# Optimization experiments

Hardware: AMD Instinct MI355X
Metric: run time of the kernel (lower is better)

Reference implementation:

```python
import jax, jax.numpy as jnp
import numpy as np

D_MODEL = 1024
N_HEADS = 16
D_HEAD = D_MODEL // N_HEADS
SCALE = D_HEAD ** -0.5


def setup_inputs() -> dict:
    key = jax.random.key(0)
    ks = jax.random.split(key, 9)
    s = 0.02
    x = jax.random.normal(ks[0], (2, 2048, D_MODEL), dtype=jnp.float32)
    Wq = jax.random.normal(ks[1], (D_MODEL, D_MODEL), dtype=jnp.float32) * s
    Wk = jax.random.normal(ks[2], (D_MODEL, D_MODEL), dtype=jnp.float32) * s
    Wv = jax.random.normal(ks[3], (D_MODEL, D_MODEL), dtype=jnp.float32) * s
    Wo = jax.random.normal(ks[4], (D_MODEL, D_MODEL), dtype=jnp.float32) * s
    bq = jax.random.normal(ks[5], (D_MODEL,), dtype=jnp.float32) * s
    bk = jax.random.normal(ks[6], (D_MODEL,), dtype=jnp.float32) * s
    bv = jax.random.normal(ks[7], (D_MODEL,), dtype=jnp.float32) * s
    bo = jax.random.normal(ks[8], (D_MODEL,), dtype=jnp.float32) * s
    return {"x": x, "Wq": Wq, "bq": bq, "Wk": Wk, "bk": bk,
            "Wv": Wv, "bv": bv, "Wo": Wo, "bo": bo}


def reference(x, Wq, bq, Wk, bk, Wv, bv, Wo, bo):
    B, S, _ = x.shape
    # torch nn.Linear: y = x @ W.T + b
    def proj(W, b):
        h = jnp.einsum('bsd,ed->bse', x, W) + b
        return h.reshape(B, S, N_HEADS, D_HEAD).transpose(0, 2, 1, 3)  # [B,H,S,Dh]
    Q = proj(Wq, bq)
    K = proj(Wk, bk)
    V = proj(Wv, bv)
    # chunked QK^T softmax over full K == full attention (no mask, dropout=0)
    scores = jnp.einsum('bhqd,bhkd->bhqk', Q, K) * SCALE  # [B,H,S,S]
    attn = jax.nn.softmax(scores, axis=-1)
    out = jnp.einsum('bhqk,bhkd->bhqd', attn, V)
    out = out.transpose(0, 2, 1, 3).reshape(B, S, D_MODEL)
    return jnp.einsum('bsd,ed->bse', out, Wo) + bo
```

## Files before the change

### kernel.cpp

```cpp
#include <hip/hip_runtime.h>
#include <cstdint>
#include <cstddef>


typedef unsigned short u16;
typedef unsigned int u32;
typedef __bf16 bf16x8 __attribute__((ext_vector_type(8)));
typedef float f32x4 __attribute__((ext_vector_type(4)));

#define GLOAD_LDS16(gp, lp)                                                            \
  __builtin_amdgcn_global_load_lds((const __attribute__((address_space(1))) void*)(gp),\
                                   (__attribute__((address_space(3))) void*)(lp),      \
                                   16, 0, 0)

__device__ __forceinline__ u16 f2bf(float f) {
  unsigned u = __builtin_bit_cast(unsigned, f);
  u = u + 0x7fffu + ((u >> 16) & 1u);
  return (u16)(u >> 16);
}

__device__ __forceinline__ u32 cvtpk(float a, float b) {
  u32 r;
  asm("v_cvt_pk_bf16_f32 %0, %1, %2" : "=v"(r) : "v"(a), "v"(b));
  return r;
}

#define QSCALE 0.1803368801111204f

__global__ void cvt_all(const float* __restrict__ x,
                        const float* __restrict__ wq, const float* __restrict__ wk,
                        const float* __restrict__ wv, const float* __restrict__ wo,
                        u16* __restrict__ xb, u16* __restrict__ wqb,
                        u16* __restrict__ wkb, u16* __restrict__ wvb,
                        u16* __restrict__ wob) {
  int bx = blockIdx.x;
  const float* s; u16* d; int off;
  if (bx < 2048)      { s = x;  d = xb;  off = bx; }
  else if (bx < 2560) { s = wq; d = wqb; off = bx - 2048; }
  else if (bx < 3072) { s = wk; d = wkb; off = bx - 2560; }
  else if (bx < 3584) { s = wv; d = wvb; off = bx - 3072; }
  else                { s = wo; d = wob; off = bx - 3584; }
  int i = off * 2048 + threadIdx.x * 8;
  float4 a = *(const float4*)(s + i);
  float4 b = *(const float4*)(s + i + 4);
  uint4 o;
  o.x = f2bf(a.x) | ((u32)f2bf(a.y) << 16);
  o.y = f2bf(a.z) | ((u32)f2bf(a.w) << 16);
  o.z = f2bf(b.x) | ((u32)f2bf(b.y) << 16);
  o.w = f2bf(b.z) | ((u32)f2bf(b.w) << 16);
  *(uint4*)(d + i) = o;
}

template <int MODE, int BM, int BN>
__global__ __launch_bounds__(256, MODE == 0 ? 3 : 4) void gemm_mfma(
    const u16* __restrict__ A,
    const u16* __restrict__ W0, const u16* __restrict__ W1, const u16* __restrict__ W2,
    const float* __restrict__ b0, const float* __restrict__ b1, const float* __restrict__ b2,
    u16* __restrict__ o0, u16* __restrict__ o1, u16* __restrict__ o2,
    float* __restrict__ oF)
{
  constexpr int MF = BM / 32;
  constexpr int NF = BN / 32;
  constexpr int AG = BM / 32;
  constexpr int BG = BN / 32;
  constexpr int NY = (MODE == 0) ? 32 : 64;
  constexpr int TOT = (MODE == 0) ? 24 * 32 : 16 * 64;

  __shared__ __align__(16) u16 As[BM * 64];
  __shared__ __align__(16) u16 Bs[BN * 64];

  const int tid = threadIdx.x;
  const int w = tid >> 6, l = tid & 63;
  const int lane = l & 15, quad = l >> 4;
  const int wm = w >> 1, wn = w & 1;

  const int idb = blockIdx.y * gridDim.x + blockIdx.x;
  const int lid = (idb & 7) * (TOT >> 3) + (idb >> 3);
  const int m0 = (lid % NY) * BM;
  const int n0g = (lid / NY) * BN;

  const int src = (MODE == 0) ? (n0g >> 10) : 0;
  const u16* Wsel = (MODE == 0) ? (src == 0 ? W0 : (src == 1 ? W1 : W2)) : W0;
  const float* bsel = (MODE == 0) ? (src == 0 ? b0 : (src == 1 ? b1 : b2)) : b0;
  const int n_base = (MODE == 0) ? (n0g & 1023) : n0g;

  const int c8 = ((l & 7) ^ (l >> 3)) * 8;
  const int lrow = l >> 3;

  f32x4 acc[MF][NF] = {};

  for (int kt = 0; kt < 1024; kt += 64) {
    __syncthreads();
    const u16* Ag = A + (size_t)m0 * 1024 + kt;
    const u16* Bg = Wsel + (size_t)n_base * 1024 + kt;
    #pragma unroll
    for (int i = 0; i < AG; ++i) {
      int rr = w * (8 * AG) + i * 8;
      GLOAD_LDS16(Ag + (size_t)(rr + lrow) * 1024 + c8, As + rr * 64);
    }
    #pragma unroll
    for (int i = 0; i < BG; ++i) {
      int rr = w * (8 * BG) + i * 8;
      GLOAD_LDS16(Bg + (size_t)(rr + lrow) * 1024 + c8, Bs + rr * 64);
    }
    __syncthreads();

    bf16x8 af[MF][2], bf[NF][2];
    #pragma unroll
    for (int mf = 0; mf < MF; ++mf)
      #pragma unroll
      for (int ks = 0; ks < 2; ++ks)
        af[mf][ks] = *(const bf16x8*)((const char*)As +
            (wm * (BM / 2) + mf * 16 + lane) * 128 + (((ks * 4 + quad) ^ (lane & 7)) * 16));
    #pragma unroll
    for (int nf = 0; nf < NF; ++nf)
      #pragma unroll
      for (int ks = 0; ks < 2; ++ks)
        bf[nf][ks] = *(const bf16x8*)((const char*)Bs +
            (wn * (BN / 2) + nf * 16 + lane) * 128 + (((ks * 4 + quad) ^ (lane & 7)) * 16));
    #pragma unroll
    for (int ks = 0; ks < 2; ++ks)
      #pragma unroll
      for (int mf = 0; mf < MF; ++mf)
        #pragma unroll
        for (int nf = 0; nf < NF; ++nf)
          acc[mf][nf] = __builtin_amdgcn_mfma_f32_16x16x32_bf16(
              af[mf][ks], bf[nf][ks], acc[mf][nf], 0, 0, 0);
  }

  float bb[NF];
  #pragma unroll
  for (int nf = 0; nf < NF; ++nf)
    bb[nf] = bsel[n_base + wn * (BN / 2) + nf * 16 + lane];

  u16* osel = (MODE == 0) ? (src == 0 ? o0 : (src == 1 ? o1 : o2)) : o0;

  #pragma unroll
  for (int mf = 0; mf < MF; ++mf) {
    int mb = m0 + wm * (BM / 2) + mf * 16 + quad * 4;
    #pragma unroll
    for (int nf = 0; nf < NF; ++nf) {
      int n_l = wn * (BN / 2) + nf * 16 + lane;
      if (MODE == 0 && src != 1) {
        float sc = (src == 0) ? QSCALE : 1.0f;
        float v0 = (acc[mf][nf][0] + bb[nf]) * sc;
        float v1 = (acc[mf][nf][1] + bb[nf]) * sc;
        float v2 = (acc[mf][nf][2] + bb[nf]) * sc;
        float v3 = (acc[mf][nf][3] + bb[nf]) * sc;
        int bi = mb >> 11, s = mb & 2047;
        int n_in = n_base + n_l;
        int h = n_in >> 6, dh = n_in & 63;
        uint2 pk = make_uint2(cvtpk(v0, v1), cvtpk(v2, v3));
        *(uint2*)(osel + (((size_t)(bi * 16 + h) * 64 + dh) * 2048 + s)) = pk;
      } else {
        #pragma unroll
        for (int r = 0; r < 4; ++r) {
          float v = acc[mf][nf][r] + bb[nf];
          int m = mb + r;
          if (MODE == 0) {
            int bi = m >> 11, s = m & 2047;
            int n_in = n_base + n_l;
            int h = n_in >> 6, dh = n_in & 63;
            osel[(((size_t)(bi * 16 + h) * 2048 + s) << 6) + dh] = f2bf(v);
          } else {
            oF[(size_t)m * 1024 + n0g + n_l] = v;
          }
        }
      }
    }
  }
}

union SMemU {
  struct {
    u16 K[3][64 * 64];
    u16 V[3][64 * 64];
  } m;
  struct {
    float O[4][32 * 64];
    float L[4][32];
  } f;
};

__global__ __launch_bounds__(512, 4) void attn_mfma(
    const u16* __restrict__ Qg_, const u16* __restrict__ Kg_,
    const u16* __restrict__ VTg_, u16* __restrict__ Og)
{
  __shared__ __align__(16) SMemU sm;

  const int tid = threadIdx.x;
  const int w = tid >> 6, l = tid & 63;
  const int lane = l & 15, quad = l >> 4;
  const int g = w >> 1;
  const int kh = w & 1;

  const int idb = blockIdx.y * 16 + blockIdx.x;
  const int lid = (idb & 7) * 64 + (idb >> 3);
  const int bh = lid >> 4;
  const int q0 = (lid & 15) * 128;

  const u16* QTg = Qg_ + (size_t)bh * 64 * 2048;
  const u16* Kg  = Kg_ + (size_t)bh * 2048 * 64;
  const u16* VTg = VTg_ + (size_t)bh * 64 * 2048;

  const int c8 = ((l & 7) ^ (l >> 3)) * 8;
  const int lrow = l >> 3;
  const int rr = w * 8;

  const int qcol = q0 + g * 32 + lane;
  bf16x8 bq[2][2];
  #pragma unroll
  for (int qf = 0; qf < 2; ++qf)
    #pragma unroll
    for (int ks = 0; ks < 2; ++ks) {
      bf16x8 v;
      #pragma unroll
      for (int j = 0; j < 8; ++j)
        v[j] = __builtin_bit_cast(__bf16,
            QTg[(size_t)(ks * 32 + quad * 8 + j) * 2048 + qcol + qf * 16]);
      bq[qf][ks] = v;
    }

  GLOAD_LDS16(Kg + (size_t)(rr + lrow) * 64 + c8, sm.m.K[0] + rr * 64);
  GLOAD_LDS16(VTg + (size_t)(rr + lrow) * 2048 + c8, sm.m.V[0] + rr * 64);
  GLOAD_LDS16(Kg + (size_t)(64 + rr + lrow) * 64 + c8, sm.m.K[1] + rr * 64);
  GLOAD_LDS16(VTg + (size_t)(rr + lrow) * 2048 + 64 + c8, sm.m.V[1] + rr * 64);

  f32x4 oa[2][4] = {};
  float lsum[2] = {0.f, 0.f};
  int cur = 0;

  for (int kt = 0; kt < 32; ++kt) {
    if (kt < 31) asm volatile("s_waitcnt vmcnt(2)" ::: "memory");
    else         asm volatile("s_waitcnt vmcnt(0)" ::: "memory");
    __builtin_amdgcn_s_barrier();
    asm volatile("" ::: "memory");

    if (kt < 30) {
      int pf = (cur == 0) ? 2 : cur - 1;
      GLOAD_LDS16(Kg + (size_t)((kt + 2) * 64 + rr + lrow) * 64 + c8,
                  sm.m.K[pf] + rr * 64);
      GLOAD_LDS16(VTg + (size_t)(rr + lrow) * 2048 + (kt + 2) * 64 + c8,
                  sm.m.V[pf] + rr * 64);
    }

    f32x4 sa[2][2] = {};
    #pragma unroll
    for (int ks = 0; ks < 2; ++ks) {
      bf16x8 ak[2];
      #pragma unroll
      for (int kf = 0; kf < 2; ++kf)
        ak[kf] = *(const bf16x8*)((const char*)sm.m.K[cur] +
            (kh * 32 + kf * 16 + lane) * 128 + (((ks * 4 + quad) ^ (lane & 7)) * 16));
      #pragma unroll
      for (int kf = 0; kf < 2; ++kf)
        #pragma unroll
        for (int qf = 0; qf < 2; ++qf)
          sa[kf][qf] = __builtin_amdgcn_mfma_f32_16x16x32_bf16(
              ak[kf], bq[qf][ks], sa[kf][qf], 0, 0, 0);
    }

    bf16x8 ap[2];
    #pragma unroll
    for (int qf = 0; qf < 2; ++qf) {
      float x0 = __builtin_amdgcn_exp2f(sa[0][qf][0]);
      float x1 = __builtin_amdgcn_exp2f(sa[0][qf][1]);
      float x2 = __builtin_amdgcn_exp2f(sa[0][qf][2]);
      float x3 = __builtin_amdgcn_exp2f(sa[0][qf][3]);
      float y0 = __builtin_amdgcn_exp2f(sa[1][qf][0]);
      float y1 = __builtin_amdgcn_exp2f(sa[1][qf][1]);
      float y2 = __builtin_amdgcn_exp2f(sa[1][qf][2]);
      float y3 = __builtin_amdgcn_exp2f(sa[1][qf][3]);
      lsum[qf] += ((x0 + x1) + (x2 + x3)) + ((y0 + y1) + (y2 + y3));
      u32 X0 = cvtpk(x0, x1), X1 = cvtpk(x2, x3);
      u32 Y0 = cvtpk(y0, y1), Y1 = cvtpk(y2, y3);
      asm("v_permlane32_swap_b32 %0, %1" : "+v"(X0), "+v"(Y0));
      asm("v_permlane16_swap_b32 %0, %1" : "+v"(X0), "+v"(Y0));
      asm("v_permlane32_swap_b32 %0, %1" : "+v"(X1), "+v"(Y1));
      asm("v_permlane16_swap_b32 %0, %1" : "+v"(X1), "+v"(Y1));
      uint4 d4 = make_uint4(X0, X1, Y0, Y1);
      ap[qf] = __builtin_bit_cast(bf16x8, d4);
    }

    {
      bf16x8 bv[4];
      #pragma unroll
      for (int df = 0; df < 4; ++df)
        bv[df] = *(const bf16x8*)((const char*)sm.m.V[cur] +
            (df * 16 + lane) * 128 + (((kh * 4 + quad) ^ (lane & 7)) * 16));
      #pragma unroll
      for (int qf = 0; qf < 2; ++qf)
        #pragma unroll
        for (int df = 0; df < 4; ++df)
          oa[qf][df] = __builtin_amdgcn_mfma_f32_16x16x32_bf16(
              ap[qf], bv[df], oa[qf][df], 0, 0, 0);
    }

    cur = (cur == 2) ? 0 : cur + 1;
  }

  #pragma unroll
  for (int qf = 0; qf < 2; ++qf) {
    lsum[qf] += __shfl_xor(lsum[qf], 16);
    lsum[qf] += __shfl_xor(lsum[qf], 32);
  }

  __syncthreads();
  if (kh == 1) {
    #pragma unroll
    for (int qf = 0; qf < 2; ++qf)
      #pragma unroll
      for (int df = 0; df < 4; ++df)
        #pragma unroll
        for (int r = 0; r < 4; ++r)
          sm.f.O[g][(qf * 16 + quad * 4 + r) * 64 + df * 16 + lane] = oa[qf][df][r];
    if (l < 16) {
      sm.f.L[g][l] = lsum[0];
      sm.f.L[g][16 + l] = lsum[1];
    }
  }
  __syncthreads();
  if (kh == 0) {
    const int b = bh >> 4, hh = bh & 15;
    u16* Ob = Og + ((size_t)b * 2048 + q0 + g * 32) * 1024 + hh * 64;
    float ltot[2];
    #pragma unroll
    for (int qf = 0; qf < 2; ++qf)
      ltot[qf] = lsum[qf] + sm.f.L[g][qf * 16 + lane];
    #pragma unroll
    for (int qf = 0; qf < 2; ++qf)
      #pragma unroll
      for (int r = 0; r < 4; ++r) {
        float inv = 1.0f / __shfl(ltot[qf], quad * 4 + r, 16);
        int qrow = qf * 16 + quad * 4 + r;
        #pragma unroll
        for (int df = 0; df < 4; ++df) {
          float v = oa[qf][df][r] + sm.f.O[g][qrow * 64 + df * 16 + lane];
          Ob[(size_t)qrow * 1024 + df * 16 + lane] = f2bf(v * inv);
        }
      }
  }
}

extern "C" void kernel_launch(void* const* d_in, const int* in_sizes, int n_in,
                              void* d_out, int out_size, void* d_ws, size_t ws_size,
                              hipStream_t stream)
{
  (void)in_sizes; (void)n_in; (void)out_size; (void)ws_size;
  const float* x  = (const float*)d_in[0];
  const float* Wq = (const float*)d_in[1];
  const float* bq = (const float*)d_in[2];
  const float* Wk = (const float*)d_in[3];
  const float* bk = (const float*)d_in[4];
  const float* Wv = (const float*)d_in[5];
  const float* bv = (const float*)d_in[6];
  const float* Wo = (const float*)d_in[7];
  const float* bo = (const float*)d_in[8];
  float* y = (float*)d_out;

  const size_t NM = (size_t)4096 * 1024;
  u16* xb  = (u16*)d_ws;
  u16* wqb = xb + NM;
  u16* wkb = wqb + 1024 * 1024;
  u16* wvb = wkb + 1024 * 1024;
  u16* wob = wvb + 1024 * 1024;
  u16* Qb  = wob + 1024 * 1024;
  u16* Kb  = Qb + NM;
  u16* VTb = Kb + NM;
  u16* AOb = VTb + NM;

  cvt_all<<<4096, 256, 0, stream>>>(x, Wq, Wk, Wv, Wo, xb, wqb, wkb, wvb, wob);

  gemm_mfma<0, 128, 128><<<dim3(24, 32), 256, 0, stream>>>(
      xb, wqb, wkb, wvb, bq, bk, bv, Qb, Kb, VTb, nullptr);

  attn_mfma<<<dim3(16, 32), 512, 0, stream>>>(Qb, Kb, VTb, AOb);

  gemm_mfma<1, 64, 64><<<dim3(16, 64), 256, 0, stream>>>(
      AOb, wob, nullptr, nullptr, bo, nullptr, nullptr,
      nullptr, nullptr, nullptr, y);
}
```

Before: 179.0 us.

## Double-buffer LDS tiles in GEMM to overlap global loads with MFMA

The projection GEMM kernel now keeps two LDS buffers for the A and B tiles. It issues the global-to-LDS loads for the next K tile before computing on the current one, so there is one barrier per iteration instead of two. This is meant to hide global memory latency behind the MFMA work. It doubles the LDS footprint, and the QKV mode's occupancy hint drops from 3 to 2 blocks per CU to match.

```diff
diff --git a/kernel.cpp b/kernel.cpp
--- a/kernel.cpp
+++ b/kernel.cpp
@@ -52,7 +52,7 @@
 }
 
 template <int MODE, int BM, int BN>
-__global__ __launch_bounds__(256, MODE == 0 ? 3 : 4) void gemm_mfma(
+__global__ __launch_bounds__(256, MODE == 0 ? 2 : 4) void gemm_mfma(
     const u16* __restrict__ A,
     const u16* __restrict__ W0, const u16* __restrict__ W1, const u16* __restrict__ W2,
     const float* __restrict__ b0, const float* __restrict__ b1, const float* __restrict__ b2,
@@ -65,9 +65,10 @@
   constexpr int BG = BN / 32;
   constexpr int NY = (MODE == 0) ? 32 : 64;
   constexpr int TOT = (MODE == 0) ? 24 * 32 : 16 * 64;
-
-  __shared__ __align__(16) u16 As[BM * 64];
-  __shared__ __align__(16) u16 Bs[BN * 64];
+  constexpr int NT = 16;
+
+  __shared__ __align__(16) u16 As[2][BM * 64];
+  __shared__ __align__(16) u16 Bs[2][BN * 64];
 
   const int tid = threadIdx.x;
   const int w = tid >> 6, l = tid & 63;
@@ -87,36 +88,47 @@
   const int c8 = ((l & 7) ^ (l >> 3)) * 8;
   const int lrow = l >> 3;
 
-  f32x4 acc[MF][NF] = {};
-
-  for (int kt = 0; kt < 1024; kt += 64) {
-    __syncthreads();
-    const u16* Ag = A + (size_t)m0 * 1024 + kt;
-    const u16* Bg = Wsel + (size_t)n_base * 1024 + kt;
+  const u16* Ag0 = A + (size_t)m0 * 1024;
+  const u16* Bg0 = Wsel + (size_t)n_base * 1024;
+
+  auto stage = [&](int buf, int kt) {
+    const u16* Ag = Ag0 + kt * 64;
+    const u16* Bg = Bg0 + kt * 64;
     #pragma unroll
     for (int i = 0; i < AG; ++i) {
       int rr = w * (8 * AG) + i * 8;
-      GLOAD_LDS16(Ag + (size_t)(rr + lrow) * 1024 + c8, As + rr * 64);
+      GLOAD_LDS16(Ag + (size_t)(rr + lrow) * 1024 + c8, As[buf] + rr * 64);
     }
     #pragma unroll
     for (int i = 0; i < BG; ++i) {
       int rr = w * (8 * BG) + i * 8;
-      GLOAD_LDS16(Bg + (size_t)(rr + lrow) * 1024 + c8, Bs + rr * 64);
-    }
-    __syncthreads();
+      GLOAD_LDS16(Bg + (size_t)(rr + lrow) * 1024 + c8, Bs[buf] + rr * 64);
+    }
+  };
+
+  f32x4 acc[MF][NF] = {};
+
+  stage(0, 0);
+  asm volatile("s_waitcnt vmcnt(0)" ::: "memory");
+  __builtin_amdgcn_s_barrier();
+  asm volatile("" ::: "memory");
+
+  for (int kt = 0; kt < NT; ++kt) {
+    const int cur = kt & 1;
+    if (kt < NT - 1) stage(cur ^ 1, kt + 1);
 
     bf16x8 af[MF][2], bf[NF][2];
     #pragma unroll
     for (int mf = 0; mf < MF; ++mf)
       #pragma unroll
       for (int ks = 0; ks < 2; ++ks)
-        af[mf][ks] = *(const bf16x8*)((const char*)As +
+        af[mf][ks] = *(const bf16x8*)((const char*)As[cur] +
             (wm * (BM / 2) + mf * 16 + lane) * 128 + (((ks * 4 + quad) ^ (lane & 7)) * 16));
     #pragma unroll
     for (int nf = 0; nf < NF; ++nf)
       #pragma unroll
       for (int ks = 0; ks < 2; ++ks)
-        bf[nf][ks] = *(const bf16x8*)((const char*)Bs +
+        bf[nf][ks] = *(const bf16x8*)((const char*)Bs[cur] +
             (wn * (BN / 2) + nf * 16 + lane) * 128 + (((ks * 4 + quad) ^ (lane & 7)) * 16));
     #pragma unroll
     for (int ks = 0; ks < 2; ++ks)
@@ -126,6 +138,12 @@
         for (int nf = 0; nf < NF; ++nf)
           acc[mf][nf] = __builtin_amdgcn_mfma_f32_16x16x32_bf16(
               af[mf][ks], bf[nf][ks], acc[mf][nf], 0, 0, 0);
+
+    if (kt < NT - 1) {
+      asm volatile("s_waitcnt vmcnt(0)" ::: "memory");
+      __builtin_amdgcn_s_barrier();
+      asm volatile("" ::: "memory");
+    }
   }
 
   float bb[NF];
```

Measured after the change: 189.9 us. 6.1% more time.
